# Performance work log

Measured on AMD Instinct MI355X. Metric: run time of the kernel, lower is better.

The kernel has to match this reference:

```python
import jax, jax.numpy as jnp
import numpy as np

N_QUBITS = 10
DIM = 1 << N_QUBITS
N_PARAMS = 6 * N_QUBITS - 3
W_MUL = (2 ** 0.5) * (5 ** -0.5)  # he_std * lrmul with gain=sqrt(2), use_wscale=True, lrmul=1

_C = jnp.complex64
X = jnp.array([[0, 1], [1, 0]], dtype=_C)
Y = jnp.array([[0, -1j], [1j, 0]], dtype=_C)
Z = jnp.array([[1, 0], [0, -1]], dtype=_C)
XX = jnp.kron(X, X)
YY = jnp.kron(Y, Y)
ZZ = jnp.kron(Z, Z)
CNOT = jnp.array([[1, 0, 0, 0], [0, 1, 0, 0], [0, 0, 0, 1], [0, 0, 1, 0]], dtype=_C)


def _rot(theta, P):
    # exp(-i theta/2 P) for involutory P (X, Y, Z, XX, YY, ZZ)
    th = theta.astype(_C)
    eye = jnp.eye(P.shape[0], dtype=_C)
    return jnp.cos(th / 2) * eye - 1j * jnp.sin(th / 2) * P


def _apply(rho, G, axes):
    # contract k-qubit gate G (2^k x 2^k) onto the given tensor axes of rho
    k = len(axes)
    Gt = G.reshape((2,) * (2 * k))
    rho = jnp.tensordot(Gt, rho, axes=(list(range(k, 2 * k)), list(axes)))
    return jnp.moveaxis(rho, list(range(k)), list(axes))


def _evolve(rho_t, w):
    # rho_t: [B] + [2]*n (row qubits) + [2]*n (col qubits); implements rho -> U rho U^dagger
    n = N_QUBITS
    for q in range(n - 1):
        gates = [_rot(w[3 * q + 0], XX), _rot(w[3 * q + 1], YY), _rot(w[3 * q + 2], ZZ), CNOT]
        for G in gates:
            rho_t = _apply(rho_t, G, (1 + q, 2 + q))            # G on rows
            rho_t = _apply(rho_t, G.conj(), (1 + n + q, 2 + n + q))  # G^dagger on cols
    wl = w[3 * n - 3:]
    for q in range(n):
        # ZYXLayer: rz, ry, rx per wire
        gates = [_rot(wl[3 * q + 0], Z), _rot(wl[3 * q + 1], Y), _rot(wl[3 * q + 2], X)]
        for G in gates:
            rho_t = _apply(rho_t, G, (1 + q,))
            rho_t = _apply(rho_t, G.conj(), (1 + n + q,))
    return rho_t


def setup_inputs() -> dict:
    key = jax.random.key(0)
    k1, k2, k3 = jax.random.split(key, 3)
    B = 16
    return {
        'x_real': jax.random.normal(k1, (B, 1, DIM), dtype=jnp.float32),
        'x_imag': jax.random.normal(k2, (B, 1, DIM), dtype=jnp.float32),
        'weight': jax.random.uniform(k3, (N_PARAMS,), dtype=jnp.float32, minval=0.0, maxval=2 * np.pi),
        'dimA': 5,
    }


def reference(x_real, x_imag, weight, dimA):
    x = (x_real + 1j * x_imag).astype(_C)              # [B, 1, DIM]
    B = x.shape[0]
    w = weight * W_MUL
    rho = jnp.einsum('boi,boj->bij', x, x.conj())      # |x><x| : [B, DIM, DIM]
    rho_t = rho.reshape((B,) + (2,) * (2 * N_QUBITS))
    rho_t = _evolve(rho_t, w)
    rho = rho_t.reshape(B, DIM, DIM)
    dimB = N_QUBITS - dimA
    dA, dB = 1 << dimA, 1 << dimB
    r = rho.reshape(B, dB, dA, dB, dA)
    red = jnp.einsum('biaic->bac', r)                  # partial trace over first dimB qubits
    return red.reshape(B, 1, dA * dA)
```

## Files before the change

kernel.cpp:

```cpp
#include <hip/hip_runtime.h>

#define NQ   10
#define DIM  1024
#define NP   57
#define WMUL 0.6324555320336759f

__global__ __launch_bounds__(256) void qupool_sv_kernel(
    const float* __restrict__ xr,
    const float* __restrict__ xi,
    const float* __restrict__ w,
    const int*   __restrict__ dimA_p,
    float* __restrict__ out,
    int out_size)
{
    __shared__ float sre[DIM];
    __shared__ float sim[DIM];
    __shared__ float sc[NP], ss[NP];

    const int b = blockIdx.x;
    const int t = threadIdx.x;

    if (t < NP) {
        float th = w[t] * (WMUL * 0.5f);
        sc[t] = cosf(th);
        ss[t] = sinf(th);
    }
    for (int j = t; j < DIM; j += 256) {
        sre[j] = xr[b * DIM + j];
        sim[j] = xi[b * DIM + j];
    }
    __syncthreads();

    for (int q = 0; q < NQ - 1; ++q) {
        const int p  = NQ - 1 - q;
        const int pl = p - 1;
        const float c1 = sc[3*q],   s1 = ss[3*q];
        const float c2 = sc[3*q+1], s2 = ss[3*q+1];
        const float c3 = sc[3*q+2], s3 = ss[3*q+2];

        const int g    = t;
        const int low  = g & ((1 << pl) - 1);
        const int high = g >> pl;
        const int i0   = (high << (p + 1)) | low;
        const int i1   = i0 | (1 << pl);
        const int i2   = i0 | (1 << p);
        const int i3   = i2 | (1 << pl);

        float r0 = sre[i0], m0 = sim[i0];
        float r1 = sre[i1], m1 = sim[i1];
        float r2 = sre[i2], m2 = sim[i2];
        float r3 = sre[i3], m3 = sim[i3];

        float t0r = c1*r0 + s1*m3, t0m = c1*m0 - s1*r3;
        float t3r = c1*r3 + s1*m0, t3m = c1*m3 - s1*r0;
        float t1r = c1*r1 + s1*m2, t1m = c1*m1 - s1*r2;
        float t2r = c1*r2 + s1*m1, t2m = c1*m2 - s1*r1;

        r0 = c2*t0r - s2*t3m; m0 = c2*t0m + s2*t3r;
        r3 = c2*t3r - s2*t0m; m3 = c2*t3m + s2*t0r;
        r1 = c2*t1r + s2*t2m; m1 = c2*t1m - s2*t2r;
        r2 = c2*t2r + s2*t1m; m2 = c2*t2m - s2*t1r;

        t0r = c3*r0 + s3*m0; t0m = c3*m0 - s3*r0;
        t3r = c3*r3 + s3*m3; t3m = c3*m3 - s3*r3;
        t1r = c3*r1 - s3*m1; t1m = c3*m1 + s3*r1;
        t2r = c3*r2 - s3*m2; t2m = c3*m2 + s3*r2;

        sre[i0] = t0r; sim[i0] = t0m;
        sre[i1] = t1r; sim[i1] = t1m;
        sre[i2] = t3r; sim[i2] = t3m;
        sre[i3] = t2r; sim[i3] = t2m;
        __syncthreads();
    }

    for (int q = 0; q < NQ; ++q) {
        const int p = NQ - 1 - q;
        const float cz = sc[27 + 3*q],     szn = ss[27 + 3*q];
        const float cy = sc[27 + 3*q + 1], sy  = ss[27 + 3*q + 1];
        const float cx = sc[27 + 3*q + 2], sx  = ss[27 + 3*q + 2];

        for (int g = t; g < DIM / 2; g += 256) {
            const int low  = g & ((1 << p) - 1);
            const int high = g >> p;
            const int i0   = (high << (p + 1)) | low;
            const int i1   = i0 | (1 << p);

            float ur = sre[i0], ui = sim[i0];
            float vr = sre[i1], vi = sim[i1];

            float tur = cz*ur + szn*ui, tui = cz*ui - szn*ur;
            float tvr = cz*vr - szn*vi, tvi = cz*vi + szn*vr;
            ur = cy*tur - sy*tvr; ui = cy*tui - sy*tvi;
            vr = sy*tur + cy*tvr; vi = sy*tui + cy*tvi;
            tur = cx*ur + sx*vi; tui = cx*ui - sx*vr;
            tvr = cx*vr + sx*ui; tvi = cx*vi - sx*ur;

            sre[i0] = tur; sim[i0] = tui;
            sre[i1] = tvr; sim[i1] = tvi;
        }
        __syncthreads();
    }

    const int dimA = dimA_p[0];
    const int dA   = 1 << dimA;
    const int dB   = DIM >> dimA;
    const int nout = dA * dA;
    const bool cplx = (out_size >= 2 * (int)gridDim.x * nout);

    for (int o = t; o < nout; o += 256) {
        const int a = o / dA;
        const int c = o % dA;
        float accr = 0.f, acci = 0.f;
        for (int i = 0; i < dB; ++i) {
            const int ia = i * dA + a;
            const int ic = i * dA + c;
            const float ar = sre[ia], ai = sim[ia];
            const float cr = sre[ic], ci = sim[ic];
            accr += ar * cr + ai * ci;
            acci += ai * cr - ar * ci;
        }
        const size_t oo = (size_t)b * nout + o;
        if (cplx) {
            out[2 * oo]     = accr;
            out[2 * oo + 1] = acci;
        } else {
            out[oo] = accr;
        }
    }
}

extern "C" void kernel_launch(void* const* d_in, const int* in_sizes, int n_in,
                              void* d_out, int out_size, void* d_ws, size_t ws_size,
                              hipStream_t stream) {
    const float* xr = (const float*)d_in[0];
    const float* xi = (const float*)d_in[1];
    const float* w  = (const float*)d_in[2];
    const int*   dA = (const int*)d_in[3];
    float* out = (float*)d_out;

    const int B = in_sizes[0] / DIM;
    qupool_sv_kernel<<<dim3(B), dim3(256), 0, stream>>>(xr, xi, w, dA, out, out_size);
}
```

Before: 70.14 us.

## Fuse first gate into load, pair 1q layers, swizzle float2 LDS, specialize trace

After: 67.23 us. 4.1% less time.

```diff
diff --git a/kernel.cpp b/kernel.cpp
--- a/kernel.cpp
+++ b/kernel.cpp
@@ -4,6 +4,36 @@
 #define DIM  1024
 #define NP   57
 #define WMUL 0.6324555320336759f
+
+__device__ __forceinline__ int ixs(int i) { return i ^ ((i >> 4) & 15); }
+
+__device__ __forceinline__ void chain1q(float2& u, float2& v,
+    float cz, float sz, float cy, float sy, float cx, float sx)
+{
+    float tur = cz*u.x + sz*u.y, tui = cz*u.y - sz*u.x;
+    float tvr = cz*v.x - sz*v.y, tvi = cz*v.y + sz*v.x;
+    float ur = cy*tur - sy*tvr, ui = cy*tui - sy*tvi;
+    float vr = sy*tur + cy*tvr, vi = sy*tui + cy*tvi;
+    u.x = cx*ur + sx*vi; u.y = cx*ui - sx*vr;
+    v.x = cx*vr + sx*ui; v.y = cx*vi - sx*ur;
+}
+
+__device__ __forceinline__ void gate2q(float2& A0, float2& A1, float2& A2, float2& A3,
+    float c1, float s1, float c2, float s2, float c3, float s3)
+{
+    float t0r = c1*A0.x + s1*A3.y, t0m = c1*A0.y - s1*A3.x;
+    float t3r = c1*A3.x + s1*A0.y, t3m = c1*A3.y - s1*A0.x;
+    float t1r = c1*A1.x + s1*A2.y, t1m = c1*A1.y - s1*A2.x;
+    float t2r = c1*A2.x + s1*A1.y, t2m = c1*A2.y - s1*A1.x;
+    float r0 = c2*t0r - s2*t3m, m0 = c2*t0m + s2*t3r;
+    float r3 = c2*t3r - s2*t0m, m3 = c2*t3m + s2*t0r;
+    float r1 = c2*t1r + s2*t2m, m1 = c2*t1m - s2*t2r;
+    float r2 = c2*t2r + s2*t1m, m2 = c2*t2m - s2*t1r;
+    A0.x = c3*r0 + s3*m0; A0.y = c3*m0 - s3*r0;
+    A3.x = c3*r3 + s3*m3; A3.y = c3*m3 - s3*r3;
+    A1.x = c3*r1 - s3*m1; A1.y = c3*m1 + s3*r1;
+    A2.x = c3*r2 - s3*m2; A2.y = c3*m2 + s3*r2;
+}
 
 __global__ __launch_bounds__(256) void qupool_sv_kernel(
     const float* __restrict__ xr,
@@ -13,118 +43,132 @@
     float* __restrict__ out,
     int out_size)
 {
-    __shared__ float sre[DIM];
-    __shared__ float sim[DIM];
+    __shared__ float2 s[DIM];
     __shared__ float sc[NP], ss[NP];
 
     const int b = blockIdx.x;
     const int t = threadIdx.x;
+    const int base = b * DIM;
 
+    float c1, s1, c2, s2, c3, s3;
+    {
+        float th0 = w[0] * (WMUL * 0.5f);
+        float th1 = w[1] * (WMUL * 0.5f);
+        float th2 = w[2] * (WMUL * 0.5f);
+        sincosf(th0, &s1, &c1);
+        sincosf(th1, &s2, &c2);
+        sincosf(th2, &s3, &c3);
+    }
     if (t < NP) {
         float th = w[t] * (WMUL * 0.5f);
-        sc[t] = cosf(th);
-        ss[t] = sinf(th);
+        float sv, cv; sincosf(th, &sv, &cv);
+        sc[t] = cv; ss[t] = sv;
     }
-    for (int j = t; j < DIM; j += 256) {
-        sre[j] = xr[b * DIM + j];
-        sim[j] = xi[b * DIM + j];
+
+    {
+        float2 A0 = make_float2(xr[base + t      ], xi[base + t      ]);
+        float2 A1 = make_float2(xr[base + t + 256], xi[base + t + 256]);
+        float2 A2 = make_float2(xr[base + t + 512], xi[base + t + 512]);
+        float2 A3 = make_float2(xr[base + t + 768], xi[base + t + 768]);
+        gate2q(A0, A1, A2, A3, c1, s1, c2, s2, c3, s3);
+        s[ixs(t      )] = A0;
+        s[ixs(t + 256)] = A1;
+        s[ixs(t + 512)] = A3;
+        s[ixs(t + 768)] = A2;
     }
     __syncthreads();
 
-    for (int q = 0; q < NQ - 1; ++q) {
+    #pragma unroll
+    for (int q = 1; q < NQ - 1; ++q) {
         const int p  = NQ - 1 - q;
         const int pl = p - 1;
-        const float c1 = sc[3*q],   s1 = ss[3*q];
-        const float c2 = sc[3*q+1], s2 = ss[3*q+1];
-        const float c3 = sc[3*q+2], s3 = ss[3*q+2];
+        const float g1c = sc[3*q  ], g1s = ss[3*q  ];
+        const float g2c = sc[3*q+1], g2s = ss[3*q+1];
+        const float g3c = sc[3*q+2], g3s = ss[3*q+2];
 
-        const int g    = t;
-        const int low  = g & ((1 << pl) - 1);
-        const int high = g >> pl;
+        const int low  = t & ((1 << pl) - 1);
+        const int high = t >> pl;
         const int i0   = (high << (p + 1)) | low;
         const int i1   = i0 | (1 << pl);
         const int i2   = i0 | (1 << p);
         const int i3   = i2 | (1 << pl);
 
-        float r0 = sre[i0], m0 = sim[i0];
-        float r1 = sre[i1], m1 = sim[i1];
-        float r2 = sre[i2], m2 = sim[i2];
-        float r3 = sre[i3], m3 = sim[i3];
-
-        float t0r = c1*r0 + s1*m3, t0m = c1*m0 - s1*r3;
-        float t3r = c1*r3 + s1*m0, t3m = c1*m3 - s1*r0;
-        float t1r = c1*r1 + s1*m2, t1m = c1*m1 - s1*r2;
-        float t2r = c1*r2 + s1*m1, t2m = c1*m2 - s1*r1;
-
-        r0 = c2*t0r - s2*t3m; m0 = c2*t0m + s2*t3r;
-        r3 = c2*t3r - s2*t0m; m3 = c2*t3m + s2*t0r;
-        r1 = c2*t1r + s2*t2m; m1 = c2*t1m - s2*t2r;
-        r2 = c2*t2r + s2*t1m; m2 = c2*t2m - s2*t1r;
-
-        t0r = c3*r0 + s3*m0; t0m = c3*m0 - s3*r0;
-        t3r = c3*r3 + s3*m3; t3m = c3*m3 - s3*r3;
-        t1r = c3*r1 - s3*m1; t1m = c3*m1 + s3*r1;
-        t2r = c3*r2 - s3*m2; t2m = c3*m2 + s3*r2;
-
-        sre[i0] = t0r; sim[i0] = t0m;
-        sre[i1] = t1r; sim[i1] = t1m;
-        sre[i2] = t3r; sim[i2] = t3m;
-        sre[i3] = t2r; sim[i3] = t2m;
+        float2 A0 = s[ixs(i0)], A1 = s[ixs(i1)], A2 = s[ixs(i2)], A3 = s[ixs(i3)];
+        gate2q(A0, A1, A2, A3, g1c, g1s, g2c, g2s, g3c, g3s);
+        s[ixs(i0)] = A0; s[ixs(i1)] = A1;
+        s[ixs(i2)] = A3; s[ixs(i3)] = A2;
         __syncthreads();
     }
 
-    for (int q = 0; q < NQ; ++q) {
-        const int p = NQ - 1 - q;
-        const float cz = sc[27 + 3*q],     szn = ss[27 + 3*q];
-        const float cy = sc[27 + 3*q + 1], sy  = ss[27 + 3*q + 1];
-        const float cx = sc[27 + 3*q + 2], sx  = ss[27 + 3*q + 2];
+    #pragma unroll
+    for (int j = 0; j < 5; ++j) {
+        const int bl = 8 - 2*j;
+        const int bh = bl + 1;
+        const int kb = 27 + 6*j;
+        const float cz0 = sc[kb+0], sz0 = ss[kb+0];
+        const float cy0 = sc[kb+1], sy0 = ss[kb+1];
+        const float cx0 = sc[kb+2], sx0 = ss[kb+2];
+        const float cz1 = sc[kb+3], sz1 = ss[kb+3];
+        const float cy1 = sc[kb+4], sy1 = ss[kb+4];
+        const float cx1 = sc[kb+5], sx1 = ss[kb+5];
 
-        for (int g = t; g < DIM / 2; g += 256) {
-            const int low  = g & ((1 << p) - 1);
-            const int high = g >> p;
-            const int i0   = (high << (p + 1)) | low;
-            const int i1   = i0 | (1 << p);
+        const int low  = t & ((1 << bl) - 1);
+        const int high = t >> bl;
+        const int i0   = (high << (bh + 1)) | low;
+        const int i1   = i0 | (1 << bl);
+        const int i2   = i0 | (1 << bh);
+        const int i3   = i2 | (1 << bl);
 
-            float ur = sre[i0], ui = sim[i0];
-            float vr = sre[i1], vi = sim[i1];
-
-            float tur = cz*ur + szn*ui, tui = cz*ui - szn*ur;
-            float tvr = cz*vr - szn*vi, tvi = cz*vi + szn*vr;
-            ur = cy*tur - sy*tvr; ui = cy*tui - sy*tvi;
-            vr = sy*tur + cy*tvr; vi = sy*tui + cy*tvi;
-            tur = cx*ur + sx*vi; tui = cx*ui - sx*vr;
-            tvr = cx*vr + sx*ui; tvi = cx*vi - sx*ur;
-
-            sre[i0] = tur; sim[i0] = tui;
-            sre[i1] = tvr; sim[i1] = tvi;
-        }
+        float2 A0 = s[ixs(i0)], A1 = s[ixs(i1)], A2 = s[ixs(i2)], A3 = s[ixs(i3)];
+        chain1q(A0, A2, cz0, sz0, cy0, sy0, cx0, sx0);
+        chain1q(A1, A3, cz0, sz0, cy0, sy0, cx0, sx0);
+        chain1q(A0, A1, cz1, sz1, cy1, sy1, cx1, sx1);
+        chain1q(A2, A3, cz1, sz1, cy1, sy1, cx1, sx1);
+        s[ixs(i0)] = A0; s[ixs(i1)] = A1; s[ixs(i2)] = A2; s[ixs(i3)] = A3;
         __syncthreads();
     }
 
     const int dimA = dimA_p[0];
     const int dA   = 1 << dimA;
-    const int dB   = DIM >> dimA;
     const int nout = dA * dA;
     const bool cplx = (out_size >= 2 * (int)gridDim.x * nout);
 
-    for (int o = t; o < nout; o += 256) {
-        const int a = o / dA;
-        const int c = o % dA;
-        float accr = 0.f, acci = 0.f;
-        for (int i = 0; i < dB; ++i) {
-            const int ia = i * dA + a;
-            const int ic = i * dA + c;
-            const float ar = sre[ia], ai = sim[ia];
-            const float cr = sre[ic], ci = sim[ic];
-            accr += ar * cr + ai * ci;
-            acci += ai * cr - ar * ci;
+    if (dA == 32) {
+        const int c  = t & 31;
+        const int a0 = t >> 5;
+        float ar[4]  = {0.f, 0.f, 0.f, 0.f};
+        float aim[4] = {0.f, 0.f, 0.f, 0.f};
+        #pragma unroll 4
+        for (int iB = 0; iB < 32; ++iB) {
+            const float2 vc = s[ixs(iB*32 + c)];
+            #pragma unroll
+            for (int k = 0; k < 4; ++k) {
+                const float2 va = s[ixs(iB*32 + a0 + 8*k)];
+                ar[k]  += va.x*vc.x + va.y*vc.y;
+                aim[k] += va.y*vc.x - va.x*vc.y;
+            }
         }
-        const size_t oo = (size_t)b * nout + o;
-        if (cplx) {
-            out[2 * oo]     = accr;
-            out[2 * oo + 1] = acci;
-        } else {
-            out[oo] = accr;
+        #pragma unroll
+        for (int k = 0; k < 4; ++k) {
+            const size_t oo = (size_t)b*nout + (t + 256*k);
+            if (cplx) { out[2*oo] = ar[k]; out[2*oo+1] = aim[k]; }
+            else      { out[oo] = ar[k]; }
+        }
+    } else {
+        const int dB = DIM >> dimA;
+        for (int o = t; o < nout; o += 256) {
+            const int a = o >> dimA;
+            const int c = o & (dA - 1);
+            float accr = 0.f, acci = 0.f;
+            for (int i = 0; i < dB; ++i) {
+                const float2 va = s[ixs(i*dA + a)];
+                const float2 vv = s[ixs(i*dA + c)];
+                accr += va.x*vv.x + va.y*vv.y;
+                acci += va.y*vv.x - va.x*vv.y;
+            }
+            const size_t oo = (size_t)b*nout + o;
+            if (cplx) { out[2*oo] = accr; out[2*oo+1] = acci; }
+            else      { out[oo] = accr; }
         }
     }
 }
```
